# Performance work log

Measured on AMD Instinct MI355X. Metric: run time of the kernel, lower is better.

## Reference

```python
import jax, jax.numpy as jnp
import numpy as np

ARITY = 2
DEPTH = 11          # full tree: levels 0..DEPTH, leaves at DEPTH
H = 1024
V = 32001           # vocab_size + 1 (null token)


def _preorder_perm(depth, arity):
    """Permutation mapping pre-order position -> BFS (level-concatenated) index."""
    offsets = np.concatenate([[0], np.cumsum(arity ** np.arange(depth + 1))])
    order = []
    def rec(d, p):
        order.append(int(offsets[d] + p))
        if d < depth:
            for c in range(arity):
                rec(d + 1, p * arity + c)
    rec(0, 0)
    return np.asarray(order, dtype=np.int32)

_PERM = _preorder_perm(DEPTH, ARITY)


def setup_inputs() -> dict:
    key = jax.random.key(0)
    ks = jax.random.split(key, 9)
    s = 0.02  # small init scale for numerical sanity
    return {
        "root_hidden": jax.random.normal(ks[0], (H,), jnp.float32),
        "W1v": jax.random.normal(ks[1], (H, 2 * H), jnp.float32) * s,
        "b1v": jax.random.normal(ks[2], (2 * H,), jnp.float32) * s,
        "W2v": jax.random.normal(ks[3], (2 * H, V), jnp.float32) * s,
        "b2v": jax.random.normal(ks[4], (V,), jnp.float32) * s,
        "W1c": jax.random.normal(ks[5], (H, 2 * H), jnp.float32) * s,
        "b1c": jax.random.normal(ks[6], (2 * H,), jnp.float32) * s,
        "W2c": jax.random.normal(ks[7], (2 * H, ARITY * H), jnp.float32) * s,
        "b2c": jax.random.normal(ks[8], (ARITY * H,), jnp.float32) * s,
    }


def _mlp(h, W1, b1, W2, b2):
    # Linear -> Sigmoid -> Linear (matches nn.Sequential in the torch module)
    return jax.nn.sigmoid(h @ W1 + b1) @ W2 + b2


def reference(root_hidden, W1v, b1v, W2v, b2v, W1c, b1c, W2c, b2c):
    # Level-wise vectorized sweep over the full tree (batches all nodes at a depth).
    h = root_hidden[None, :]                  # [1, H]
    prods = []
    for d in range(DEPTH + 1):
        prods.append(_mlp(h, W1v, b1v, W2v, b2v))     # [a^d, V]
        if d < DEPTH:
            # to_children then split into arity children per node
            h = _mlp(h, W1c, b1c, W2c, b2c).reshape(-1, H)  # [a^(d+1), H]
    raw = jnp.concatenate(prods, axis=0)      # BFS order, [N, V]
    raw = raw[_PERM]                          # reorder to pre-order (torch recursion order)
    return jax.nn.log_softmax(raw, axis=1)
```

## Files before the change

kernel.cpp:

```cpp
#include <hip/hip_runtime.h>
#include <hip/hip_bf16.h>

#define DEPTH_T 11
#define HDIM 1024
#define VDIM 32001
#define NNODES 4095
#define LDV 32008

typedef __attribute__((ext_vector_type(8))) short bf16x8;
typedef __attribute__((ext_vector_type(8))) unsigned short ushort8;
typedef __attribute__((ext_vector_type(4))) float floatx4;
typedef __attribute__((ext_vector_type(2))) long longx2;

__device__ __forceinline__ int preorder_pos(int m) {
    int q = m + 1;
    int d = 31 - __clz(q);
    int pos = 0;
    for (int i = 1; i <= d; ++i) {
        int b = (q >> (d - i)) & 1;
        pos += 1 + b * ((1 << (DEPTH_T - i + 1)) - 1);
    }
    return pos;
}

__device__ __forceinline__ float bf2f(unsigned short u) {
    return __uint_as_float(((unsigned)u) << 16);
}

__device__ __forceinline__ unsigned char f2e4m3(float v) {
    return (unsigned char)(__builtin_amdgcn_cvt_pk_fp8_f32(v, v, 0, false) & 0xff);
}

#define BM 128
#define BN 128
#define BK 32

template<int MODE, bool SWAPG>
__global__ __launch_bounds__(256, 2) void gemm_bt(
    const __hip_bfloat16* __restrict__ A,
    const __hip_bfloat16* __restrict__ Bt,
    const float* __restrict__ bias,
    void* __restrict__ outp,
    int M, int N, int K, int ldout)
{
    __shared__ __align__(16) __hip_bfloat16 As[BM][BK];
    __shared__ __align__(16) __hip_bfloat16 Bs[BN][BK];

    const int tid  = threadIdx.x;
    const int wave = tid >> 6;
    const int lane = tid & 63;
    const int m0 = (SWAPG ? blockIdx.x : blockIdx.y) * BM;
    const int n0 = (SWAPG ? blockIdx.y : blockIdx.x) * BN;
    const int wm = (wave & 1) * 64;
    const int wn = (wave >> 1) * 64;

    floatx4 acc[4][4];
#pragma unroll
    for (int i = 0; i < 4; ++i)
#pragma unroll
        for (int j = 0; j < 4; ++j) acc[i][j] = (floatx4)0.0f;

    const int lrow = lane >> 2;
    const int lcol = (lane & 3) * 8;
    const int fr = lane & 15;
    const int fk = (lane >> 4) * 8;

    for (int k0 = 0; k0 < K; k0 += BK) {
        __syncthreads();
#pragma unroll
        for (int t = 0; t < 2; ++t) {
            const int r = (wave * 2 + t) * 16;
            int gm = m0 + r + lrow; gm = gm < M ? gm : M - 1;
            const __hip_bfloat16* gp = A + (size_t)gm * K + (k0 + lcol);
            __builtin_amdgcn_global_load_lds(
                (const __attribute__((address_space(1))) void*)gp,
                (__attribute__((address_space(3))) void*)(&As[r][0]),
                16, 0, 0);
        }
#pragma unroll
        for (int t = 0; t < 2; ++t) {
            const int r = (wave * 2 + t) * 16;
            int gn = n0 + r + lrow; gn = gn < N ? gn : N - 1;
            const __hip_bfloat16* gp = Bt + (size_t)gn * K + (k0 + lcol);
            __builtin_amdgcn_global_load_lds(
                (const __attribute__((address_space(1))) void*)gp,
                (__attribute__((address_space(3))) void*)(&Bs[r][0]),
                16, 0, 0);
        }
        __syncthreads();

        bf16x8 af[4], bfv[4];
#pragma unroll
        for (int i = 0; i < 4; ++i)
            af[i] = *(const bf16x8*)(&As[wm + i * 16 + fr][fk]);
#pragma unroll
        for (int j = 0; j < 4; ++j)
            bfv[j] = *(const bf16x8*)(&Bs[wn + j * 16 + fr][fk]);
#pragma unroll
        for (int i = 0; i < 4; ++i)
#pragma unroll
            for (int j = 0; j < 4; ++j)
                acc[i][j] = __builtin_amdgcn_mfma_f32_16x16x32_bf16(
                    af[i], bfv[j], acc[i][j], 0, 0, 0);
    }

    const int rq = (lane >> 4) * 4;
    if (MODE == 2 || MODE == 3) {
#pragma unroll
        for (int i = 0; i < 4; ++i) {
#pragma unroll
            for (int r = 0; r < 4; ++r) {
                const int gm = m0 + wm + i * 16 + rq + r;
                if (gm >= M) continue;
                const size_t orow = (size_t)preorder_pos(gm) * ldout;
#pragma unroll
                for (int j = 0; j < 4; ++j) {
                    const int gn = n0 + wn + j * 16 + fr;
                    if (gn < N) {
                        float v = acc[i][j][r] + bias[gn];
                        if (MODE == 2) ((float*)outp)[orow + gn] = v;
                        else ((__hip_bfloat16*)outp)[orow + gn] = __float2bfloat16(v);
                    }
                }
            }
        }
    } else {
#pragma unroll
        for (int i = 0; i < 4; ++i) {
#pragma unroll
            for (int r = 0; r < 4; ++r) {
                const int gm = m0 + wm + i * 16 + rq + r;
                if (gm >= M) continue;
#pragma unroll
                for (int j = 0; j < 4; ++j) {
                    const int gn = n0 + wn + j * 16 + fr;
                    if (gn < N) {
                        float v = acc[i][j][r] + bias[gn];
                        if (MODE != 1) v = 1.0f / (1.0f + __expf(-v));
                        if (MODE == 4)
                            ((unsigned char*)outp)[(size_t)gm * ldout + gn] = f2e4m3(v);
                        else
                            ((__hip_bfloat16*)outp)[(size_t)gm * ldout + gn] = __float2bfloat16(v);
                    }
                }
            }
        }
    }
}

#define B2M 256
#define B2N 256

__global__ __launch_bounds__(512, 2) void gemm256_f8(
    const unsigned char* __restrict__ A,
    const unsigned char* __restrict__ Bt,
    const float* __restrict__ bias,
    __hip_bfloat16* __restrict__ outp,
    int M, int N, int K, int ldout)
{
    __shared__ __align__(16) char smem[131072];

    const int tid  = threadIdx.x;
    const int wave = tid >> 6;
    const int lane = tid & 63;

    const int nwy = (N + B2N - 1) / B2N;
    int mt, nt;
    {
        const int g = blockIdx.x >> 8;
        const int i = blockIdx.x & 255;
        const int k = i & 7, s = i >> 3;
        mt = (k & 1) * 4 + (s & 3) + (g & 1) * 8;
        nt = (k >> 1) * 8 + (s >> 2) + (g >> 1) * 32;
    }
    if (nt >= nwy) return;
    const int m0 = mt * B2M;
    const int n0 = nt * B2N;

    const int wm = (wave >> 2) * 128;
    const int wn = (wave & 3) * 64;
    const int nkt = K >> 7;

    const int s_row = lane >> 3;
    const int s_col = ((lane & 7) ^ s_row) * 16;

    const int fr  = lane & 15;
    const int fkq = lane >> 4;
    const int swz = (fr & 7) << 4;
    const int c0  = (fkq * 16) ^ swz;
    const int c1  = (64 + fkq * 16) ^ swz;
    const int aoff = (wm + fr) * 128;
    const int boff = 32768 + (wn + fr) * 128;

    floatx4 acc[8][4];
#pragma unroll
    for (int i = 0; i < 8; ++i)
#pragma unroll
        for (int j = 0; j < 4; ++j) acc[i][j] = (floatx4)0.0f;

    longx2 a0[8], a1[8], b0[4], b1[4];

    auto mkb = [&](const unsigned char* gb, int g0, int lim, int h, int inst) {
        int gr = g0 + h * 128 + (inst * 8 + wave) * 8 + s_row;
        gr = gr < lim ? gr : lim - 1;
        return gb + (size_t)gr * K + s_col;
    };
    const unsigned char* pA00 = mkb(A,  m0, M, 0, 0);
    const unsigned char* pA01 = mkb(A,  m0, M, 0, 1);
    const unsigned char* pA10 = mkb(A,  m0, M, 1, 0);
    const unsigned char* pA11 = mkb(A,  m0, M, 1, 1);
    const unsigned char* pB00 = mkb(Bt, n0, N, 0, 0);
    const unsigned char* pB01 = mkb(Bt, n0, N, 0, 1);
    const unsigned char* pB10 = mkb(Bt, n0, N, 1, 0);
    const unsigned char* pB11 = mkb(Bt, n0, N, 1, 1);

#define STAGE(bsel, mat, h, PP0, PP1, kt) do { \
    const int ko_ = ((kt) < nkt ? (kt) : 0) * 128; \
    __builtin_amdgcn_global_load_lds( \
        (const __attribute__((address_space(1))) void*)((PP0) + ko_), \
        (__attribute__((address_space(3))) void*) \
            (smem + (bsel)*65536 + (mat)*32768 + (h)*16384 + wave*1024), 16, 0, 0); \
    __builtin_amdgcn_global_load_lds( \
        (const __attribute__((address_space(1))) void*)((PP1) + ko_), \
        (__attribute__((address_space(3))) void*) \
            (smem + (bsel)*65536 + (mat)*32768 + (h)*16384 + 8192 + wave*1024), 16, 0, 0); \
} while (0)

#define RD_A(dst, bsel, cc) \
    _Pragma("unroll") \
    for (int i = 0; i < 8; ++i) \
        dst[i] = *(const longx2*)(smem + (bsel) * 65536 + aoff + i * 2048 + (cc));
#define RD_B(dst, bsel, cc) \
    _Pragma("unroll") \
    for (int j = 0; j < 4; ++j) \
        dst[j] = *(const longx2*)(smem + (bsel) * 65536 + boff + j * 2048 + (cc));
#define MM(ib, AA, BB) \
    _Pragma("unroll") \
    for (int i = 0; i < 4; ++i) \
    _Pragma("unroll") \
    for (int j = 0; j < 4; ++j) { \
        acc[(ib) + i][j] = __builtin_amdgcn_mfma_f32_16x16x32_fp8_fp8( \
            AA[(ib) + i][0], BB[j][0], acc[(ib) + i][j], 0, 0, 0); \
        acc[(ib) + i][j] = __builtin_amdgcn_mfma_f32_16x16x32_fp8_fp8( \
            AA[(ib) + i][1], BB[j][1], acc[(ib) + i][j], 0, 0, 0); \
    }
#define LGKM0  asm volatile("s_waitcnt lgkmcnt(0)" ::: "memory")
#define VM4    asm volatile("s_waitcnt vmcnt(4)" ::: "memory")
#define BAR    __builtin_amdgcn_s_barrier()
#define PRIO1  __builtin_amdgcn_s_setprio(1)
#define PRIO0  __builtin_amdgcn_s_setprio(0)

    STAGE(0, 0, 0, pA00, pA01, 0);
    STAGE(0, 0, 1, pA10, pA11, 0);
    STAGE(0, 1, 0, pB00, pB01, 0);
    STAGE(0, 1, 1, pB10, pB11, 0);
    STAGE(1, 0, 0, pA00, pA01, 1);
    STAGE(1, 0, 1, pA10, pA11, 1);
    VM4;
    BAR;

#pragma unroll 1
    for (int t = 0; t < nkt; t += 2) {
        RD_A(a0, 0, c0); RD_B(b0, 0, c0);
        STAGE(1, 1, 0, pB00, pB01, t + 1);
        BAR; LGKM0;
        PRIO1; MM(0, a0, b0); PRIO0;
        BAR;
        RD_A(a1, 0, c1); RD_B(b1, 0, c1);
        STAGE(1, 1, 1, pB10, pB11, t + 1);
        BAR; LGKM0;
        PRIO1; MM(4, a0, b0); PRIO0;
        BAR;
        STAGE(0, 0, 0, pA00, pA01, t + 2);
        BAR;
        PRIO1; MM(0, a1, b1); PRIO0;
        BAR;
        STAGE(0, 0, 1, pA10, pA11, t + 2);
        VM4;
        BAR;
        PRIO1; MM(4, a1, b1); PRIO0;
        BAR;
        RD_A(a0, 1, c0); RD_B(b0, 1, c0);
        STAGE(0, 1, 0, pB00, pB01, t + 2);
        BAR; LGKM0;
        PRIO1; MM(0, a0, b0); PRIO0;
        BAR;
        RD_A(a1, 1, c1); RD_B(b1, 1, c1);
        STAGE(0, 1, 1, pB10, pB11, t + 2);
        BAR; LGKM0;
        PRIO1; MM(4, a0, b0); PRIO0;
        BAR;
        STAGE(1, 0, 0, pA00, pA01, t + 3);
        BAR;
        PRIO1; MM(0, a1, b1); PRIO0;
        BAR;
        STAGE(1, 0, 1, pA10, pA11, t + 3);
        VM4;
        BAR;
        PRIO1; MM(4, a1, b1); PRIO0;
        BAR;
    }

#undef STAGE
#undef RD_A
#undef RD_B
#undef MM
#undef LGKM0
#undef VM4
#undef BAR
#undef PRIO1
#undef PRIO0

    const int rq = (lane >> 4) * 4;
#pragma unroll
    for (int i = 0; i < 8; ++i) {
#pragma unroll
        for (int r = 0; r < 4; ++r) {
            const int gm = m0 + wm + i * 16 + rq + r;
            if (gm >= M) continue;
            const size_t orow = (size_t)preorder_pos(gm) * ldout;
#pragma unroll
            for (int j = 0; j < 4; ++j) {
                const int gn = n0 + wn + j * 16 + fr;
                if (gn < N) {
                    float v = acc[i][j][r] + bias[gn];
                    outp[orow + gn] = __float2bfloat16(v);
                }
            }
        }
    }
}

template<int MODE>
__global__ __launch_bounds__(256) void gemm_small(
    const __hip_bfloat16* __restrict__ A,
    const __hip_bfloat16* __restrict__ Bt,
    const float* __restrict__ bias,
    __hip_bfloat16* __restrict__ O,
    int M, int N, int K)
{
    const int wave = threadIdx.x >> 6, lane = threadIdx.x & 63;
    const int n0 = blockIdx.x * 64 + wave * 16;
    const int m0 = blockIdx.y * 16;
    const int fr = lane & 15, fk = (lane >> 4) * 8;

    int am = m0 + fr; am = am < M ? am : M - 1;
    const __hip_bfloat16* ap = A + (size_t)am * K + fk;
    const __hip_bfloat16* bp = Bt + (size_t)(n0 + fr) * K + fk;

    floatx4 acc = (floatx4)0.0f;
#pragma unroll 8
    for (int k0 = 0; k0 < K; k0 += 32) {
        bf16x8 av = *(const bf16x8*)(ap + k0);
        bf16x8 bv = *(const bf16x8*)(bp + k0);
        acc = __builtin_amdgcn_mfma_f32_16x16x32_bf16(av, bv, acc, 0, 0, 0);
    }

    const int rq = (lane >> 4) * 4;
    const int gn = n0 + fr;
    const float b = bias[gn];
#pragma unroll
    for (int r = 0; r < 4; ++r) {
        const int gm = m0 + rq + r;
        if (gm >= M) continue;
        float v = acc[r] + b;
        if (MODE == 0) v = 1.0f / (1.0f + __expf(-v));
        O[(size_t)gm * N + gn] = __float2bfloat16(v);
    }
}

__global__ __launch_bounds__(256) void transpose_to_bf16(
    const float* __restrict__ in, __hip_bfloat16* __restrict__ outT, int R, int C)
{
    __shared__ float tile[64][65];
    const int c0 = blockIdx.x * 64, r0 = blockIdx.y * 64;
    const int tx = threadIdx.x & 63, ty = threadIdx.x >> 6;
#pragma unroll
    for (int i = 0; i < 64; i += 4) {
        int r = r0 + ty + i, c = c0 + tx;
        tile[ty + i][tx] = (r < R && c < C) ? in[(size_t)r * C + c] : 0.0f;
    }
    __syncthreads();
#pragma unroll
    for (int i = 0; i < 64; i += 4) {
        int rr = c0 + ty + i, cc = r0 + tx;
        if (rr < C && cc < R) outT[(size_t)rr * R + cc] = __float2bfloat16(tile[tx][ty + i]);
    }
}

__global__ __launch_bounds__(256) void transpose_to_fp8(
    const float* __restrict__ in, unsigned char* __restrict__ outT, int R, int C)
{
    __shared__ float tile[64][65];
    const int c0 = blockIdx.x * 64, r0 = blockIdx.y * 64;
    const int tx = threadIdx.x & 63, ty = threadIdx.x >> 6;
#pragma unroll
    for (int i = 0; i < 64; i += 4) {
        int r = r0 + ty + i, c = c0 + tx;
        tile[ty + i][tx] = (r < R && c < C) ? in[(size_t)r * C + c] : 0.0f;
    }
    __syncthreads();
    const int u0 = threadIdx.x >> 4;
    const int v  = (threadIdx.x & 15) * 4;
#pragma unroll
    for (int i = 0; i < 64; i += 16) {
        const int u  = u0 + i;
        const int rr = c0 + u;
        const int cc = r0 + v;
        if (rr >= C) continue;
        if (cc + 3 < R) {
            uchar4 pk;
            pk.x = f2e4m3(tile[v + 0][u]);
            pk.y = f2e4m3(tile[v + 1][u]);
            pk.z = f2e4m3(tile[v + 2][u]);
            pk.w = f2e4m3(tile[v + 3][u]);
            *(uchar4*)(outT + (size_t)rr * R + cc) = pk;
        } else {
#pragma unroll
            for (int q = 0; q < 4; ++q)
                if (cc + q < R) outT[(size_t)rr * R + cc + q] = f2e4m3(tile[v + q][u]);
        }
    }
}

__global__ __launch_bounds__(256) void convert_root(
    const float* __restrict__ in, __hip_bfloat16* __restrict__ out)
{
    int i = blockIdx.x * 256 + threadIdx.x;
    if (i < HDIM) out[i] = __float2bfloat16(in[i]);
}

__global__ __launch_bounds__(256) void logsoftmax_bf16(
    const unsigned short* __restrict__ L, float* __restrict__ O)
{
    extern __shared__ char smem[];
    unsigned short* rb = (unsigned short*)smem;
    float* wred = (float*)(smem + 64016);
    const int tid = threadIdx.x, lane = tid & 63, wv = tid >> 6;
    const unsigned short* src = L + (size_t)blockIdx.x * LDV;

    float m = -3.0e38f;
    for (int j = tid * 8; j < 32000; j += 2048) {
        ushort8 u = *(const ushort8*)(src + j);
        *(ushort8*)(rb + j) = u;
#pragma unroll
        for (int t = 0; t < 8; ++t) m = fmaxf(m, bf2f(u[t]));
    }
    if (tid == 0) { unsigned short u = src[32000]; rb[32000] = u; m = fmaxf(m, bf2f(u)); }
#pragma unroll
    for (int off = 32; off; off >>= 1) m = fmaxf(m, __shfl_xor(m, off, 64));
    if (lane == 0) wred[wv] = m;
    __syncthreads();
    const float M4 = fmaxf(fmaxf(wred[0], wred[1]), fmaxf(wred[2], wred[3]));

    float s = 0.0f;
    for (int j = tid * 8; j < 32000; j += 2048) {
        ushort8 u = *(const ushort8*)(rb + j);
#pragma unroll
        for (int t = 0; t < 8; ++t) s += __expf(bf2f(u[t]) - M4);
    }
    if (tid == 0) s += __expf(bf2f(rb[32000]) - M4);
#pragma unroll
    for (int off = 32; off; off >>= 1) s += __shfl_xor(s, off, 64);
    if (lane == 0) wred[4 + wv] = s;
    __syncthreads();
    const float lse = M4 + __logf(wred[4] + wred[5] + wred[6] + wred[7]);

    float* dst = O + (size_t)blockIdx.x * VDIM;
    for (int j = tid * 8; j < 32000; j += 2048) {
        ushort8 u = *(const ushort8*)(rb + j);
#pragma unroll
        for (int t = 0; t < 8; ++t) dst[j + t] = bf2f(u[t]) - lse;
    }
    if (tid == 0) dst[32000] = bf2f(rb[32000]) - lse;
}

__global__ __launch_bounds__(256) void logsoftmax_rows(float* __restrict__ O, int n)
{
    __shared__ float sm[256], ssum[256];
    const int tid = threadIdx.x;
    float* p = O + (size_t)blockIdx.x * n;
    float m = -3.0e38f, s = 0.0f;
    for (int j = tid; j < n; j += 256) {
        float x = p[j];
        float nm = fmaxf(m, x);
        s = s * __expf(m - nm) + __expf(x - nm);
        m = nm;
    }
    sm[tid] = m; ssum[tid] = s;
    __syncthreads();
    for (int off = 128; off > 0; off >>= 1) {
        if (tid < off) {
            float m2 = sm[tid + off], s2 = ssum[tid + off];
            float nm = fmaxf(sm[tid], m2);
            ssum[tid] = ssum[tid] * __expf(sm[tid] - nm) + s2 * __expf(m2 - nm);
            sm[tid] = nm;
        }
        __syncthreads();
    }
    const float lse = sm[0] + __logf(ssum[0]);
    for (int j = tid; j < n; j += 256) p[j] -= lse;
}

extern "C" void kernel_launch(void* const* d_in, const int* in_sizes, int n_in,
                              void* d_out, int out_size, void* d_ws, size_t ws_size,
                              hipStream_t stream)
{
    const float* root = (const float*)d_in[0];
    const float* W1v  = (const float*)d_in[1];
    const float* b1v  = (const float*)d_in[2];
    const float* W2v  = (const float*)d_in[3];
    const float* b2v  = (const float*)d_in[4];
    const float* W1c  = (const float*)d_in[5];
    const float* b1c  = (const float*)d_in[6];
    const float* W2c  = (const float*)d_in[7];
    const float* b2c  = (const float*)d_in[8];

    char* ws = (char*)d_ws;
    __hip_bfloat16* Hall = (__hip_bfloat16*)(ws + 0);
    __hip_bfloat16* X1   = (__hip_bfloat16*)(ws +   8388608ull);
    unsigned char*  X1_8 = (unsigned char*)(ws +   8388608ull);
    __hip_bfloat16* Tt   = (__hip_bfloat16*)(ws +  25165824ull);
    __hip_bfloat16* W1vT = (__hip_bfloat16*)(ws +  29360128ull);
    __hip_bfloat16* W1cT = (__hip_bfloat16*)(ws +  33554432ull);
    __hip_bfloat16* W2cT = (__hip_bfloat16*)(ws +  37748736ull);
    __hip_bfloat16* W2vT = (__hip_bfloat16*)(ws +  46137344ull);
    unsigned char*  W2vT8= (unsigned char*)(ws +  46137344ull);
    __hip_bfloat16* Lb   = (__hip_bfloat16*)(ws + 177213440ull);
    const bool bf16_logits = ws_size >= 177213440ull + (size_t)NNODES * LDV * 2;

    dim3 blk(256);

    transpose_to_bf16<<<dim3( 32, 16), blk, 0, stream>>>(W1v, W1vT, 1024, 2048);
    if (bf16_logits)
        transpose_to_fp8<<<dim3(501, 32), blk, 0, stream>>>(W2v, W2vT8, 2048, VDIM);
    else
        transpose_to_bf16<<<dim3(501, 32), blk, 0, stream>>>(W2v, W2vT, 2048, VDIM);
    transpose_to_bf16<<<dim3( 32, 16), blk, 0, stream>>>(W1c, W1cT, 1024, 2048);
    transpose_to_bf16<<<dim3( 32, 32), blk, 0, stream>>>(W2c, W2cT, 2048, 2048);
    convert_root<<<dim3(4), blk, 0, stream>>>(root, Hall);

    for (int d = 0; d < DEPTH_T; ++d) {
        const int Md = 1 << d;
        __hip_bfloat16* Hd = Hall + (size_t)(Md - 1) * HDIM;
        __hip_bfloat16* Hn = Hall + (size_t)((2 << d) - 1) * HDIM;
        if (Md <= 256) {
            dim3 g(32, (Md + 15) / 16);
            gemm_small<0><<<g, blk, 0, stream>>>(Hd, W1cT, b1c, Tt, Md, 2048, 1024);
            gemm_small<1><<<g, blk, 0, stream>>>(Tt, W2cT, b2c, Hn, Md, 2048, 2048);
        } else {
            dim3 g(16, Md / 128);
            gemm_bt<0, false><<<g, blk, 0, stream>>>(Hd, W1cT, b1c, Tt, Md, 2048, 1024, 2048);
            gemm_bt<1, false><<<g, blk, 0, stream>>>(Tt, W2cT, b2c, Hn, Md, 2048, 2048, 2048);
        }
    }

    if (bf16_logits) {
        gemm_bt<4, false><<<dim3(16, 32), blk, 0, stream>>>(Hall, W1vT, b1v, X1_8, NNODES, 2048, 1024, 2048);
        gemm256_f8<<<dim3(2048), dim3(512), 0, stream>>>(X1_8, W2vT8, b2v, Lb, NNODES, VDIM, 2048, LDV);
        logsoftmax_bf16<<<dim3(NNODES), blk, 64048, stream>>>((const unsigned short*)Lb, (float*)d_out);
    } else {
        gemm_bt<0, false><<<dim3(16, 32), blk, 0, stream>>>(Hall, W1vT, b1v, X1, NNODES, 2048, 1024, 2048);
        gemm_bt<2, true><<<dim3(32, 251), blk, 0, stream>>>(X1, W2vT, b2v, d_out, NNODES, VDIM, 2048, VDIM);
        logsoftmax_rows<<<dim3(NNODES), blk, 0, stream>>>((float*)d_out, VDIM);
    }
}
```

Baseline: 1.364 ms.

## Load A fragments directly from global and stage only B in LDS

The fp8 256x256 GEMM stops staging the A tile through shared memory. Each lane now reads its A MFMA fragments straight from global memory into registers, while only B is double-buffered in LDS via global_load_lds with a simpler one-k-tile-per-iteration pipeline. This halves LDS use (128KB to 64KB) and cuts LDS traffic and barriers. In exchange, A reads become uncached-in-LDS global loads that are repeated by the 4 waves sharing rows, and their latency is exposed inside the loop. The STAGEB destination now adds a per-lane offset to global_load_lds, which may conflict with its wave-uniform LDS addressing semantics.

```diff
diff --git a/kernel.cpp b/kernel.cpp
--- a/kernel.cpp
+++ b/kernel.cpp
@@ -158,7 +158,7 @@
     __hip_bfloat16* __restrict__ outp,
     int M, int N, int K, int ldout)
 {
-    __shared__ __align__(16) char smem[131072];
+    __shared__ __align__(16) char smem[65536];
 
     const int tid  = threadIdx.x;
     const int wave = tid >> 6;
@@ -189,8 +189,7 @@
     const int swz = (fr & 7) << 4;
     const int c0  = (fkq * 16) ^ swz;
     const int c1  = (64 + fkq * 16) ^ swz;
-    const int aoff = (wm + fr) * 128;
-    const int boff = 32768 + (wn + fr) * 128;
+    const int boff = (wn + fr) * 128;
 
     floatx4 acc[8][4];
 #pragma unroll
@@ -198,115 +197,89 @@
 #pragma unroll
         for (int j = 0; j < 4; ++j) acc[i][j] = (floatx4)0.0f;
 
-    longx2 a0[8], a1[8], b0[4], b1[4];
-
-    auto mkb = [&](const unsigned char* gb, int g0, int lim, int h, int inst) {
-        int gr = g0 + h * 128 + (inst * 8 + wave) * 8 + s_row;
-        gr = gr < lim ? gr : lim - 1;
-        return gb + (size_t)gr * K + s_col;
+    longx2 av[8], bv[4];
+
+    const unsigned char* abase[8];
+#pragma unroll
+    for (int i = 0; i < 8; ++i) {
+        int gr = m0 + wm + i * 16 + fr; gr = gr < M ? gr : M - 1;
+        abase[i] = A + (size_t)gr * K + fkq * 16;
+    }
+
+    auto mkb = [&](int h, int inst) {
+        int gr = n0 + h * 128 + (inst * 8 + wave) * 8 + s_row;
+        gr = gr < N ? gr : N - 1;
+        return Bt + (size_t)gr * K + s_col;
     };
-    const unsigned char* pA00 = mkb(A,  m0, M, 0, 0);
-    const unsigned char* pA01 = mkb(A,  m0, M, 0, 1);
-    const unsigned char* pA10 = mkb(A,  m0, M, 1, 0);
-    const unsigned char* pA11 = mkb(A,  m0, M, 1, 1);
-    const unsigned char* pB00 = mkb(Bt, n0, N, 0, 0);
-    const unsigned char* pB01 = mkb(Bt, n0, N, 0, 1);
-    const unsigned char* pB10 = mkb(Bt, n0, N, 1, 0);
-    const unsigned char* pB11 = mkb(Bt, n0, N, 1, 1);
-
-#define STAGE(bsel, mat, h, PP0, PP1, kt) do { \
+    const unsigned char* pB00 = mkb(0, 0);
+    const unsigned char* pB01 = mkb(0, 1);
+    const unsigned char* pB10 = mkb(1, 0);
+    const unsigned char* pB11 = mkb(1, 1);
+
+#define GLD(PP, DST) \
+    __builtin_amdgcn_global_load_lds( \
+        (const __attribute__((address_space(1))) void*)(PP), \
+        (__attribute__((address_space(3))) void*)(DST), 16, 0, 0)
+#define STAGEB(bsel, kt) do { \
     const int ko_ = ((kt) < nkt ? (kt) : 0) * 128; \
-    __builtin_amdgcn_global_load_lds( \
-        (const __attribute__((address_space(1))) void*)((PP0) + ko_), \
-        (__attribute__((address_space(3))) void*) \
-            (smem + (bsel)*65536 + (mat)*32768 + (h)*16384 + wave*1024), 16, 0, 0); \
-    __builtin_amdgcn_global_load_lds( \
-        (const __attribute__((address_space(1))) void*)((PP1) + ko_), \
-        (__attribute__((address_space(3))) void*) \
-            (smem + (bsel)*65536 + (mat)*32768 + (h)*16384 + 8192 + wave*1024), 16, 0, 0); \
+    GLD(pB00 + ko_, smem + (bsel)*32768 +         wave*1024 + (lane & 63)*16); \
+    GLD(pB01 + ko_, smem + (bsel)*32768 +  8192 + wave*1024 + (lane & 63)*16); \
+    GLD(pB10 + ko_, smem + (bsel)*32768 + 16384 + wave*1024 + (lane & 63)*16); \
+    GLD(pB11 + ko_, smem + (bsel)*32768 + 24576 + wave*1024 + (lane & 63)*16); \
 } while (0)
 
-#define RD_A(dst, bsel, cc) \
+#define LD_A(koff) \
     _Pragma("unroll") \
     for (int i = 0; i < 8; ++i) \
-        dst[i] = *(const longx2*)(smem + (bsel) * 65536 + aoff + i * 2048 + (cc));
-#define RD_B(dst, bsel, cc) \
+        av[i] = *(const longx2*)(abase[i] + (koff));
+#define RD_B(bsel, cc) \
     _Pragma("unroll") \
     for (int j = 0; j < 4; ++j) \
-        dst[j] = *(const longx2*)(smem + (bsel) * 65536 + boff + j * 2048 + (cc));
-#define MM(ib, AA, BB) \
+        bv[j] = *(const longx2*)(smem + (bsel) * 32768 + boff + j * 2048 + (cc));
+#define MM_H(IB) \
     _Pragma("unroll") \
     for (int i = 0; i < 4; ++i) \
     _Pragma("unroll") \
     for (int j = 0; j < 4; ++j) { \
-        acc[(ib) + i][j] = __builtin_amdgcn_mfma_f32_16x16x32_fp8_fp8( \
-            AA[(ib) + i][0], BB[j][0], acc[(ib) + i][j], 0, 0, 0); \
-        acc[(ib) + i][j] = __builtin_amdgcn_mfma_f32_16x16x32_fp8_fp8( \
-            AA[(ib) + i][1], BB[j][1], acc[(ib) + i][j], 0, 0, 0); \
+        acc[(IB) + i][j] = __builtin_amdgcn_mfma_f32_16x16x32_fp8_fp8( \
+            av[(IB) + i][0], bv[j][0], acc[(IB) + i][j], 0, 0, 0); \
+        acc[(IB) + i][j] = __builtin_amdgcn_mfma_f32_16x16x32_fp8_fp8( \
+            av[(IB) + i][1], bv[j][1], acc[(IB) + i][j], 0, 0, 0); \
     }
 #define LGKM0  asm volatile("s_waitcnt lgkmcnt(0)" ::: "memory")
-#define VM4    asm volatile("s_waitcnt vmcnt(4)" ::: "memory")
+#define VMC4   asm volatile("s_waitcnt vmcnt(4)" ::: "memory")
+#define SB0    __builtin_amdgcn_sched_barrier(0)
 #define BAR    __builtin_amdgcn_s_barrier()
 #define PRIO1  __builtin_amdgcn_s_setprio(1)
 #define PRIO0  __builtin_amdgcn_s_setprio(0)
 
-    STAGE(0, 0, 0, pA00, pA01, 0);
-    STAGE(0, 0, 1, pA10, pA11, 0);
-    STAGE(0, 1, 0, pB00, pB01, 0);
-    STAGE(0, 1, 1, pB10, pB11, 0);
-    STAGE(1, 0, 0, pA00, pA01, 1);
-    STAGE(1, 0, 1, pA10, pA11, 1);
-    VM4;
-    BAR;
+    STAGEB(0, 0);
 
 #pragma unroll 1
-    for (int t = 0; t < nkt; t += 2) {
-        RD_A(a0, 0, c0); RD_B(b0, 0, c0);
-        STAGE(1, 1, 0, pB00, pB01, t + 1);
-        BAR; LGKM0;
-        PRIO1; MM(0, a0, b0); PRIO0;
+    for (int t = 0; t < nkt; ++t) {
+        const int cur = t & 1;
+        const int ko = t * 128;
+        LD_A(ko);
+        STAGEB(cur ^ 1, t + 1);
+        VMC4; BAR;
+        RD_B(cur, c0);
+        LGKM0; SB0;
+        PRIO1; MM_H(0); MM_H(4); PRIO0;
+        LD_A(ko + 64);
+        RD_B(cur, c1);
+        LGKM0; SB0;
+        PRIO1; MM_H(0); MM_H(4); PRIO0;
         BAR;
-        RD_A(a1, 0, c1); RD_B(b1, 0, c1);
-        STAGE(1, 1, 1, pB10, pB11, t + 1);
-        BAR; LGKM0;
-        PRIO1; MM(4, a0, b0); PRIO0;
-        BAR;
-        STAGE(0, 0, 0, pA00, pA01, t + 2);
-        BAR;
-        PRIO1; MM(0, a1, b1); PRIO0;
-        BAR;
-        STAGE(0, 0, 1, pA10, pA11, t + 2);
-        VM4;
-        BAR;
-        PRIO1; MM(4, a1, b1); PRIO0;
-        BAR;
-        RD_A(a0, 1, c0); RD_B(b0, 1, c0);
-        STAGE(0, 1, 0, pB00, pB01, t + 2);
-        BAR; LGKM0;
-        PRIO1; MM(0, a0, b0); PRIO0;
-        BAR;
-        RD_A(a1, 1, c1); RD_B(b1, 1, c1);
-        STAGE(0, 1, 1, pB10, pB11, t + 2);
-        BAR; LGKM0;
-        PRIO1; MM(4, a0, b0); PRIO0;
-        BAR;
-        STAGE(1, 0, 0, pA00, pA01, t + 3);
-        BAR;
-        PRIO1; MM(0, a1, b1); PRIO0;
-        BAR;
-        STAGE(1, 0, 1, pA10, pA11, t + 3);
-        VM4;
-        BAR;
-        PRIO1; MM(4, a1, b1); PRIO0;
-        BAR;
-    }
-
-#undef STAGE
-#undef RD_A
+    }
+
+#undef GLD
+#undef STAGEB
+#undef LD_A
 #undef RD_B
-#undef MM
+#undef MM_H
 #undef LGKM0
-#undef VM4
+#undef VMC4
+#undef SB0
 #undef BAR
 #undef PRIO1
 #undef PRIO0
```

New measurement: 1.661 ms. 1.22x slower.
